# Optimization experiments

Measured on AMD Instinct MI355X. Metric: run time of the kernel, lower is better.

## Reference

```python
import jax, jax.numpy as jnp
import numpy as np

B, D_IN, HID, DIM, M = 4096, 128, 200, 256, 32
SIGMA, OMEGA = 1.0, 1.7
LB, UB = 0.0, 1.0


def setup_inputs() -> dict:
    key = jax.random.key(0)
    ks = jax.random.split(key, 9)
    s = lambda d: 1.0 / jnp.sqrt(jnp.float32(d))
    return {
        "x": jax.random.normal(ks[0], (B, D_IN), jnp.float32),
        "b": jax.random.uniform(ks[1], (B, M), jnp.float32),
        "W1": jax.random.normal(ks[2], (D_IN, HID), jnp.float32) * s(D_IN),
        "b1": jnp.zeros((HID,), jnp.float32),
        "W2": jax.random.normal(ks[3], (HID, HID), jnp.float32) * s(HID),
        "b2": jnp.zeros((HID,), jnp.float32),
        "W3": jax.random.normal(ks[4], (HID, DIM), jnp.float32) * s(HID),
        "b3": jnp.zeros((DIM,), jnp.float32),
        "A": jax.random.normal(ks[5], (M, DIM), jnp.float32) * s(DIM),
        "step": 1000,
        "n_iter": 100,
    }


def reference(x, b, W1, b1, W2, b2, W3, b3, A, step, n_iter):
    # --- MLP: Dense(200) -> relu -> Dense(200) -> relu -> Dense(dim) ---
    h = jax.nn.relu(x @ W1 + b1)
    h = jax.nn.relu(h @ W2 + b2)
    y = h @ W3 + b3  # [B, DIM]

    # schedule = linear_schedule(0.0, 0.0, ...) -> alpha == 0.0 always
    alpha = jnp.float32(0.0)

    # --- projection onto {z : A z = b, LB <= z <= UB} via relaxed
    # Douglas-Rachford / SOR fixed-point iteration (sigma/omega) ---
    AAt_inv = jnp.linalg.inv(A @ A.T + 1e-6 * jnp.eye(M, dtype=A.dtype))

    def p_aff(z):  # affine equality projection, z: [B, DIM]
        r = z @ A.T - b            # [B, M] residual
        return z - (r @ AAt_inv) @ A

    def p_box(z):
        return jnp.clip(z, LB, UB)

    def body(z, _):
        u = p_aff(z)
        v = p_box(2.0 * u - z)     # reflection then box projection
        z = z + SIGMA * OMEGA * (v - u)
        return z, None

    z0 = y  # project.get_init(x): initialize fixed point at MLP output
    z_final, _ = jax.lax.scan(body, z0, None, length=n_iter)
    proj = p_aff(z_final)

    # interpolation between raw MLP output and projection (alpha == 0)
    out = alpha * y + (1.0 - alpha) * proj
    return out
```

## Files before the change

### kernel.cpp

```cpp
#include <hip/hip_runtime.h>
#include <hip/hip_bf16.h>

typedef float    f4v    __attribute__((ext_vector_type(4)));
typedef short    short8 __attribute__((ext_vector_type(8)));
typedef unsigned u2v    __attribute__((ext_vector_type(2)));

constexpr int Bn = 4096, TR = 16;

__device__ inline unsigned cvt2(float x, float y) {
  union { __hip_bfloat162 h; unsigned u; } c;
  c.h = __float22bfloat162_rn(float2{x, y});
  return c.u;
}
__device__ inline void split_pair(float x, float y, unsigned& hp, unsigned& lp) {
  hp = cvt2(x, y);
  float hx = __uint_as_float(hp << 16);
  float hy = __uint_as_float(hp & 0xffff0000u);
  lp = cvt2(x - hx, y - hy);
}
union S8U { unsigned u[4]; short8 s; };
__device__ inline void split8(const float v[8], short8& hi, short8& lo) {
  S8U h, l;
  #pragma unroll
  for (int d = 0; d < 4; ++d) split_pair(v[2 * d], v[2 * d + 1], h.u[d], l.u[d]);
  hi = h.s; lo = l.s;
}
__device__ inline void split8p(const float* p, short8& hi, short8& lo) {
  f4v a = *(const f4v*)p, b = *(const f4v*)(p + 4);
  float v[8] = {a[0], a[1], a[2], a[3], b[0], b[1], b[2], b[3]};
  split8(v, hi, lo);
}
__device__ inline f4v mfma16(short8 a, short8 b, f4v c) {
  return __builtin_amdgcn_mfma_f32_16x16x32_bf16(a, b, c, 0, 0, 0);
}
__device__ __attribute__((always_inline)) inline f4v gdot8(
    const short8 (&ah)[8], const short8 (&al)[8],
    const short8 (&bh)[8], const short8 (&bl)[8]) {
  f4v c = {0.f, 0.f, 0.f, 0.f};
  #pragma unroll
  for (int s = 0; s < 8; ++s) {
    c = mfma16(ah[s], bh[s], c);
    c = mfma16(al[s], bh[s], c);
    c = mfma16(ah[s], bl[s], c);
  }
  return c;
}

__global__ __launch_bounds__(256) void k_prep(const float* __restrict__ A,
                                              float* __restrict__ KAT) {
  __shared__ __align__(16) float As[32 * 256];
  __shared__ float Gm[32 * 68];
  __shared__ float GinvL[32 * 32];

  const int t = threadIdx.x;
  const int lane = t & 63, wv = t >> 6, quad = lane >> 4, l15 = lane & 15;
  const int T = wv & 1, kh = wv >> 1;

  for (int i = t; i < 2048; i += 256)
    ((f4v*)As)[i] = ((const f4v*)A)[i];
  __syncthreads();

  {
    short8 afh[2][8], afl[2][8];
    #pragma unroll
    for (int tt = 0; tt < 2; ++tt)
      #pragma unroll
      for (int s = 0; s < 8; ++s)
        split8p(As + (l15 + 16 * tt) * 256 + 32 * s + 8 * quad,
                afh[tt][s], afl[tt][s]);
    f4v cg;
    if      (wv == 0) cg = gdot8(afh[0], afl[0], afh[0], afl[0]);
    else if (wv == 1) cg = gdot8(afh[1], afl[1], afh[0], afl[0]);
    else if (wv == 2) cg = gdot8(afh[0], afl[0], afh[1], afl[1]);
    else              cg = gdot8(afh[1], afl[1], afh[1], afl[1]);
    #pragma unroll
    for (int r = 0; r < 4; ++r) {
      int gi = 16 * T + 4 * quad + r, gj = 16 * kh + l15;
      Gm[gi * 68 + gj]      = cg[r] + (gi == gj ? 1e-6f : 0.f);
      Gm[gi * 68 + 32 + gj] = (gi == gj) ? 1.f : 0.f;
    }
  }
  __syncthreads();

  if (wv == 0) {
    float gcol[32];
    #pragma unroll
    for (int i = 0; i < 32; ++i) gcol[i] = Gm[i * 68 + lane];
    #pragma unroll
    for (int k = 0; k < 32; ++k) {
      float ckk  = __shfl(gcol[k], k);
      float ipiv = 1.f / ckk;
      float pivj = gcol[k] * ipiv;
      gcol[k] = pivj;
      #pragma unroll
      for (int i = 0; i < 32; ++i) {
        if (i == k) continue;
        float cki = __shfl(gcol[i], k);
        gcol[i] = fmaf(-cki, pivj, gcol[i]);
      }
    }
    if (lane >= 32) {
      #pragma unroll
      for (int i = 0; i < 32; ++i) GinvL[i * 32 + (lane - 32)] = gcol[i];
    }
  }
  __syncthreads();

  {
    float res[32];
    #pragma unroll
    for (int m = 0; m < 32; ++m) res[m] = 0.f;
    for (int p = 0; p < 32; ++p) {
      float av = As[p * 256 + t];
      #pragma unroll
      for (int m4 = 0; m4 < 8; ++m4) {
        f4v g = *(const f4v*)&GinvL[p * 32 + 4 * m4];
        res[4 * m4 + 0] = fmaf(av, g[0], res[4 * m4 + 0]);
        res[4 * m4 + 1] = fmaf(av, g[1], res[4 * m4 + 1]);
        res[4 * m4 + 2] = fmaf(av, g[2], res[4 * m4 + 2]);
        res[4 * m4 + 3] = fmaf(av, g[3], res[4 * m4 + 3]);
      }
    }
    #pragma unroll
    for (int m4 = 0; m4 < 8; ++m4) {
      f4v v = {res[4 * m4], res[4 * m4 + 1], res[4 * m4 + 2], res[4 * m4 + 3]};
      *(f4v*)&KAT[t * 32 + 4 * m4] = v;
    }
  }
}

__global__ __launch_bounds__(256, 1) void k_main(
    const float* __restrict__ x,  const float* __restrict__ bmat,
    const float* __restrict__ W1, const float* __restrict__ b1,
    const float* __restrict__ W2, const float* __restrict__ b2,
    const float* __restrict__ W3, const float* __restrict__ b3,
    const float* __restrict__ A,  const float* __restrict__ KAT,
    const int* __restrict__ n_iter_p, float* __restrict__ out) {

  __shared__ __align__(16) float smem[11328];

  const int t = threadIdx.x;
  const int lane = t & 63, wv = t >> 6, quad = lane >> 4, l15 = lane & 15;
  const int row0 = blockIdx.x * TR;

  float* xs = smem;
  float* h1 = smem + 2112;
  float* h2 = smem + 5440;
  float* ys = smem;
  unsigned* zsm = (unsigned*)smem;
  float* rb = smem + 8768 + wv * 640;

  {
    int r = t >> 4, c8 = t & 15;
    *(f4v*)&xs[r * 132 + 8 * c8]     = *(const f4v*)&x[(size_t)(row0 + r) * 128 + 8 * c8];
    *(f4v*)&xs[r * 132 + 8 * c8 + 4] = *(const f4v*)&x[(size_t)(row0 + r) * 128 + 8 * c8 + 4];
  }
  __syncthreads();

  {
    const int rg = wv, oc = lane;
    const bool g3 = (oc < 8);
    float acc[4][4];

    #pragma unroll
    for (int oi = 0; oi < 4; ++oi)
      #pragma unroll
      for (int r = 0; r < 4; ++r) acc[oi][r] = 0.f;
    for (int k4 = 0; k4 < 32; ++k4) {
      float xv[4][4];
      #pragma unroll
      for (int r = 0; r < 4; ++r) {
        f4v v = *(const f4v*)&xs[(4 * rg + r) * 132 + 4 * k4];
        xv[r][0] = v[0]; xv[r][1] = v[1]; xv[r][2] = v[2]; xv[r][3] = v[3];
      }
      #pragma unroll
      for (int kk = 0; kk < 4; ++kk) {
        const float* wr = W1 + (4 * k4 + kk) * 200 + oc;
        float w0 = wr[0], w1c = wr[64], w2c = wr[128];
        float w3c = g3 ? wr[192] : 0.f;
        #pragma unroll
        for (int r = 0; r < 4; ++r) {
          acc[0][r] = fmaf(xv[r][kk], w0, acc[0][r]);
          acc[1][r] = fmaf(xv[r][kk], w1c, acc[1][r]);
          acc[2][r] = fmaf(xv[r][kk], w2c, acc[2][r]);
          acc[3][r] = fmaf(xv[r][kk], w3c, acc[3][r]);
        }
      }
    }
    #pragma unroll
    for (int oi = 0; oi < 4; ++oi) {
      if (oi == 3 && !g3) continue;
      float bb = b1[oc + 64 * oi];
      #pragma unroll
      for (int r = 0; r < 4; ++r)
        h1[(4 * rg + r) * 208 + oc + 64 * oi] = fmaxf(acc[oi][r] + bb, 0.f);
    }
    __syncthreads();

    #pragma unroll
    for (int oi = 0; oi < 4; ++oi)
      #pragma unroll
      for (int r = 0; r < 4; ++r) acc[oi][r] = 0.f;
    for (int k4 = 0; k4 < 50; ++k4) {
      float xv[4][4];
      #pragma unroll
      for (int r = 0; r < 4; ++r) {
        f4v v = *(const f4v*)&h1[(4 * rg + r) * 208 + 4 * k4];
        xv[r][0] = v[0]; xv[r][1] = v[1]; xv[r][2] = v[2]; xv[r][3] = v[3];
      }
      #pragma unroll
      for (int kk = 0; kk < 4; ++kk) {
        const float* wr = W2 + (4 * k4 + kk) * 200 + oc;
        float w0 = wr[0], w1c = wr[64], w2c = wr[128];
        float w3c = g3 ? wr[192] : 0.f;
        #pragma unroll
        for (int r = 0; r < 4; ++r) {
          acc[0][r] = fmaf(xv[r][kk], w0, acc[0][r]);
          acc[1][r] = fmaf(xv[r][kk], w1c, acc[1][r]);
          acc[2][r] = fmaf(xv[r][kk], w2c, acc[2][r]);
          acc[3][r] = fmaf(xv[r][kk], w3c, acc[3][r]);
        }
      }
    }
    #pragma unroll
    for (int oi = 0; oi < 4; ++oi) {
      if (oi == 3 && !g3) continue;
      float bb = b2[oc + 64 * oi];
      #pragma unroll
      for (int r = 0; r < 4; ++r)
        h2[(4 * rg + r) * 208 + oc + 64 * oi] = fmaxf(acc[oi][r] + bb, 0.f);
    }
    __syncthreads();

    #pragma unroll
    for (int oi = 0; oi < 4; ++oi)
      #pragma unroll
      for (int r = 0; r < 4; ++r) acc[oi][r] = 0.f;
    for (int k4 = 0; k4 < 50; ++k4) {
      float xv[4][4];
      #pragma unroll
      for (int r = 0; r < 4; ++r) {
        f4v v = *(const f4v*)&h2[(4 * rg + r) * 208 + 4 * k4];
        xv[r][0] = v[0]; xv[r][1] = v[1]; xv[r][2] = v[2]; xv[r][3] = v[3];
      }
      #pragma unroll
      for (int kk = 0; kk < 4; ++kk) {
        const float* wr = W3 + (4 * k4 + kk) * 256 + oc;
        float w0 = wr[0], w1c = wr[64], w2c = wr[128], w3c = wr[192];
        #pragma unroll
        for (int r = 0; r < 4; ++r) {
          acc[0][r] = fmaf(xv[r][kk], w0, acc[0][r]);
          acc[1][r] = fmaf(xv[r][kk], w1c, acc[1][r]);
          acc[2][r] = fmaf(xv[r][kk], w2c, acc[2][r]);
          acc[3][r] = fmaf(xv[r][kk], w3c, acc[3][r]);
        }
      }
    }
    __syncthreads();
    #pragma unroll
    for (int oi = 0; oi < 4; ++oi) {
      float bb = b3[oc + 64 * oi];
      #pragma unroll
      for (int r = 0; r < 4; ++r)
        ys[(4 * rg + r) * 260 + oc + 64 * oi] = acc[oi][r] + bb;
    }
  }
  __syncthreads();

  short8 aah[2][8], aal[2][8];
  f4v binit[2];
  #pragma unroll
  for (int T = 0; T < 2; ++T) {
    #pragma unroll
    for (int s = 0; s < 8; ++s) {
      const float* ap = A + (size_t)(l15 + 16 * T) * 256 + 32 * s + 8 * quad;
      float v[8];
      #pragma unroll
      for (int j = 0; j < 8; ++j) v[j] = ap[j];
      split8(v, aah[T][s], aal[T][s]);
    }
    f4v bv = *(const f4v*)&bmat[(size_t)(row0 + l15) * 32 + 16 * T + 4 * quad];
    binit[T] = -bv;
  }

  short8 kanh[4], kanl[4];
  #pragma unroll
  for (int u = 0; u < 4; ++u) {
    const int U = 4 * wv + u;
    const float* kp = KAT + (size_t)(16 * U + l15) * 32 + 8 * quad;
    float v[8];
    #pragma unroll
    for (int j = 0; j < 8; ++j) v[j] = kp[j];
    split8(v, kanh[u], kanl[u]);
  }

  int zoff[4];
  #pragma unroll
  for (int u = 0; u < 4; ++u) {
    const int U = 4 * wv + u;
    const int qp = 2 * (U & 1) + (quad >> 1);
    zoff[u] = (((U >> 3) * 4 + ((U >> 1) & 3)) * 2) * 256
              + qp * 64 + l15 * 4 + 2 * (quad & 1);
  }

  float zr[4][4];
  #pragma unroll
  for (int u = 0; u < 4; ++u) {
    const int U = 4 * wv + u;
    f4v yv = *(const f4v*)&ys[l15 * 260 + 16 * U + 4 * quad];
    #pragma unroll
    for (int r = 0; r < 4; ++r) zr[u][r] = yv[r];
  }
  __syncthreads();
  #pragma unroll
  for (int u = 0; u < 4; ++u) {
    unsigned h0, l0, h1_, l1_;
    split_pair(zr[u][0], zr[u][1], h0, l0);
    split_pair(zr[u][2], zr[u][3], h1_, l1_);
    u2v hv; hv[0] = h0; hv[1] = h1_;
    u2v lv; lv[0] = l0; lv[1] = l1_;
    *(u2v*)&zsm[zoff[u]] = hv;
    *(u2v*)&zsm[zoff[u] + 256] = lv;
  }
  __syncthreads();

  const int niter = n_iter_p[0];
  int p = 0;

  for (int it = 0; it <= niter; ++it) {
    const unsigned* zb = zsm + p * 4096;

    f4v c0[2], c1[2];
    c0[0] = binit[0]; c0[1] = binit[1];
    c1[0] = f4v{0.f, 0.f, 0.f, 0.f};
    c1[1] = f4v{0.f, 0.f, 0.f, 0.f};
    #pragma unroll
    for (int half = 0; half < 2; ++half) {
      short8 zfh[4], zfl[4];
      #pragma unroll
      for (int q4 = 0; q4 < 4; ++q4) {
        int s = 4 * half + q4;
        zfh[q4] = *(const short8*)&zb[(s * 2 + 0) * 256 + lane * 4];
        zfl[q4] = *(const short8*)&zb[(s * 2 + 1) * 256 + lane * 4];
      }
      #pragma unroll
      for (int q4 = 0; q4 < 4; ++q4) {
        int s = 4 * half + q4;
        #pragma unroll
        for (int T = 0; T < 2; ++T) {
          f4v cc = (q4 & 1) ? c1[T] : c0[T];
          cc = mfma16(aah[T][s], zfh[q4], cc);
          cc = mfma16(aal[T][s], zfh[q4], cc);
          cc = mfma16(aah[T][s], zfl[q4], cc);
          if (q4 & 1) c1[T] = cc; else c0[T] = cc;
        }
      }
    }
    #pragma unroll
    for (int T = 0; T < 2; ++T) {
      f4v rA = c0[T] + c1[T];
      *(f4v*)&rb[l15 * 36 + 16 * T + 4 * quad] = rA;
    }
    f4v ra = *(const f4v*)&rb[l15 * 36 + 8 * quad];
    f4v rbv = *(const f4v*)&rb[l15 * 36 + 8 * quad + 4];
    float rv[8] = {ra[0], ra[1], ra[2], ra[3], rbv[0], rbv[1], rbv[2], rbv[3]};
    short8 rh, rl;
    split8(rv, rh, rl);

    f4v cB[4];
    #pragma unroll
    for (int u = 0; u < 4; ++u) {
      f4v cc = {0.f, 0.f, 0.f, 0.f};
      cc = mfma16(kanh[u], rh, cc);
      cc = mfma16(kanl[u], rh, cc);
      cc = mfma16(kanh[u], rl, cc);
      cB[u] = cc;
    }

    if (it < niter) {
      unsigned* zw = zsm + (p ^ 1) * 4096;
      #pragma unroll
      for (int u = 0; u < 4; ++u) {
        #pragma unroll
        for (int r = 0; r < 4; ++r) {
          float z = zr[u][r], wvv = cB[u][r];
          float vv = fminf(fmaxf(z - 2.f * wvv, 0.f), 1.f);
          zr[u][r] = fmaf(1.7f, vv - z + wvv, z);
        }
        unsigned h0, l0, h1_, l1_;
        split_pair(zr[u][0], zr[u][1], h0, l0);
        split_pair(zr[u][2], zr[u][3], h1_, l1_);
        u2v hv; hv[0] = h0; hv[1] = h1_;
        u2v lv; lv[0] = l0; lv[1] = l1_;
        *(u2v*)&zw[zoff[u]] = hv;
        *(u2v*)&zw[zoff[u] + 256] = lv;
      }
      __syncthreads();
      p ^= 1;
    } else {
      #pragma unroll
      for (int u = 0; u < 4; ++u) {
        const int U = 4 * wv + u;
        f4v ov;
        #pragma unroll
        for (int r = 0; r < 4; ++r) ov[r] = zr[u][r] - cB[u][r];
        *(f4v*)&out[(size_t)(row0 + l15) * 256 + 16 * U + 4 * quad] = ov;
      }
    }
  }
}

extern "C" void kernel_launch(void* const* d_in, const int* in_sizes, int n_in,
                              void* d_out, int out_size, void* d_ws, size_t ws_size,
                              hipStream_t stream) {
  const float* x    = (const float*)d_in[0];
  const float* bmat = (const float*)d_in[1];
  const float* W1   = (const float*)d_in[2];
  const float* b1   = (const float*)d_in[3];
  const float* W2   = (const float*)d_in[4];
  const float* b2   = (const float*)d_in[5];
  const float* W3   = (const float*)d_in[6];
  const float* b3   = (const float*)d_in[7];
  const float* A    = (const float*)d_in[8];
  const int*  n_it  = (const int*)d_in[10];
  float* KAT = (float*)d_ws;
  float* out = (float*)d_out;

  hipLaunchKernelGGL(k_prep, dim3(1), dim3(256), 0, stream, A, KAT);
  hipLaunchKernelGGL(k_main, dim3(Bn / TR), dim3(256), 0, stream,
                     x, bmat, W1, b1, W2, b2, W3, b3, A, KAT, n_it, out);
}
```

Before: 271.7 us.

## Run projection loop on a single wave with K fragments staged in LDS

Pre-splits the KAT matrix into bf16 hi/lo fragments in shared memory. After the MLP, only wave 0 continues, holding all 16 z tiles in registers and computing both projection GEMMs itself. This removes the per-iteration block barrier and the double-buffered z exchange. In exchange, one wave does all the second-GEMM MFMA work serially and the other three SIMDs sit idle during the loop.

```diff
diff --git a/kernel.cpp b/kernel.cpp
--- a/kernel.cpp
+++ b/kernel.cpp
@@ -4,6 +4,7 @@
 typedef float    f4v    __attribute__((ext_vector_type(4)));
 typedef short    short8 __attribute__((ext_vector_type(8)));
 typedef unsigned u2v    __attribute__((ext_vector_type(2)));
+typedef unsigned u4v    __attribute__((ext_vector_type(4)));
 
 constexpr int Bn = 4096, TR = 16;
 
@@ -18,7 +19,7 @@
   float hy = __uint_as_float(hp & 0xffff0000u);
   lp = cvt2(x - hx, y - hy);
 }
-union S8U { unsigned u[4]; short8 s; };
+union S8U { unsigned u[4]; short8 s; u4v v4; };
 __device__ inline void split8(const float v[8], short8& hi, short8& lo) {
   S8U h, l;
   #pragma unroll
@@ -137,18 +138,20 @@
     const float* __restrict__ A,  const float* __restrict__ KAT,
     const int* __restrict__ n_iter_p, float* __restrict__ out) {
 
-  __shared__ __align__(16) float smem[11328];
+  __shared__ __align__(16) float    ubuf[8768];
+  __shared__ __align__(16) unsigned zfrag[4096];
+  __shared__ __align__(16) unsigned kfh[4096];
+  __shared__ __align__(16) unsigned kfl[4096];
+  __shared__ __align__(16) float    rb[576];
 
   const int t = threadIdx.x;
   const int lane = t & 63, wv = t >> 6, quad = lane >> 4, l15 = lane & 15;
   const int row0 = blockIdx.x * TR;
 
-  float* xs = smem;
-  float* h1 = smem + 2112;
-  float* h2 = smem + 5440;
-  float* ys = smem;
-  unsigned* zsm = (unsigned*)smem;
-  float* rb = smem + 8768 + wv * 640;
+  float* xs = ubuf;
+  float* h1 = ubuf + 2112;
+  float* h2 = ubuf + 5440;
+  float* ys = ubuf;
 
   {
     int r = t >> 4, c8 = t & 15;
@@ -265,7 +268,23 @@
         ys[(4 * rg + r) * 260 + oc + 64 * oi] = acc[oi][r] + bb;
     }
   }
+
+  #pragma unroll
+  for (int u = 0; u < 4; ++u) {
+    const int U = 4 * wv + u;
+    float v[8];
+    #pragma unroll
+    for (int j = 0; j < 8; ++j)
+      v[j] = KAT[(size_t)(16 * U + l15) * 32 + 8 * quad + j];
+    S8U h, l;
+    #pragma unroll
+    for (int d = 0; d < 4; ++d) split_pair(v[2 * d], v[2 * d + 1], h.u[d], l.u[d]);
+    *(u4v*)&kfh[U * 256 + lane * 4] = h.v4;
+    *(u4v*)&kfl[U * 256 + lane * 4] = l.v4;
+  }
   __syncthreads();
+
+  if (wv != 0) return;
 
   short8 aah[2][8], aal[2][8];
   f4v binit[2];
@@ -283,127 +302,98 @@
     binit[T] = -bv;
   }
 
-  short8 kanh[4], kanl[4];
-  #pragma unroll
-  for (int u = 0; u < 4; ++u) {
-    const int U = 4 * wv + u;
-    const float* kp = KAT + (size_t)(16 * U + l15) * 32 + 8 * quad;
-    float v[8];
-    #pragma unroll
-    for (int j = 0; j < 8; ++j) v[j] = kp[j];
-    split8(v, kanh[u], kanl[u]);
-  }
-
-  int zoff[4];
-  #pragma unroll
-  for (int u = 0; u < 4; ++u) {
-    const int U = 4 * wv + u;
-    const int qp = 2 * (U & 1) + (quad >> 1);
-    zoff[u] = (((U >> 3) * 4 + ((U >> 1) & 3)) * 2) * 256
-              + qp * 64 + l15 * 4 + 2 * (quad & 1);
-  }
-
-  float zr[4][4];
-  #pragma unroll
-  for (int u = 0; u < 4; ++u) {
-    const int U = 4 * wv + u;
-    f4v yv = *(const f4v*)&ys[l15 * 260 + 16 * U + 4 * quad];
-    #pragma unroll
-    for (int r = 0; r < 4; ++r) zr[u][r] = yv[r];
-  }
-  __syncthreads();
-  #pragma unroll
-  for (int u = 0; u < 4; ++u) {
+  const int zlane = (quad >> 1) * 64 + l15 * 4 + 2 * (quad & 1);
+
+  f4v zr[16];
+  #pragma unroll
+  for (int U = 0; U < 16; ++U)
+    zr[U] = *(const f4v*)&ys[l15 * 260 + 16 * U + 4 * quad];
+  #pragma unroll
+  for (int U = 0; U < 16; ++U) {
+    const int zo = (((U >> 3) * 4 + ((U >> 1) & 3)) * 2) * 256 + (U & 1) * 128 + zlane;
     unsigned h0, l0, h1_, l1_;
-    split_pair(zr[u][0], zr[u][1], h0, l0);
-    split_pair(zr[u][2], zr[u][3], h1_, l1_);
+    split_pair(zr[U][0], zr[U][1], h0, l0);
+    split_pair(zr[U][2], zr[U][3], h1_, l1_);
     u2v hv; hv[0] = h0; hv[1] = h1_;
     u2v lv; lv[0] = l0; lv[1] = l1_;
-    *(u2v*)&zsm[zoff[u]] = hv;
-    *(u2v*)&zsm[zoff[u] + 256] = lv;
-  }
-  __syncthreads();
+    *(u2v*)&zfrag[zo] = hv;
+    *(u2v*)&zfrag[zo + 256] = lv;
+  }
 
   const int niter = n_iter_p[0];
-  int p = 0;
 
   for (int it = 0; it <= niter; ++it) {
-    const unsigned* zb = zsm + p * 4096;
+    short8 zfh[8], zfl[8];
+    #pragma unroll
+    for (int s = 0; s < 8; ++s) {
+      zfh[s] = *(const short8*)&zfrag[(s * 2 + 0) * 256 + lane * 4];
+      zfl[s] = *(const short8*)&zfrag[(s * 2 + 1) * 256 + lane * 4];
+    }
 
     f4v c0[2], c1[2];
     c0[0] = binit[0]; c0[1] = binit[1];
     c1[0] = f4v{0.f, 0.f, 0.f, 0.f};
     c1[1] = f4v{0.f, 0.f, 0.f, 0.f};
     #pragma unroll
-    for (int half = 0; half < 2; ++half) {
-      short8 zfh[4], zfl[4];
-      #pragma unroll
-      for (int q4 = 0; q4 < 4; ++q4) {
-        int s = 4 * half + q4;
-        zfh[q4] = *(const short8*)&zb[(s * 2 + 0) * 256 + lane * 4];
-        zfl[q4] = *(const short8*)&zb[(s * 2 + 1) * 256 + lane * 4];
-      }
-      #pragma unroll
-      for (int q4 = 0; q4 < 4; ++q4) {
-        int s = 4 * half + q4;
-        #pragma unroll
-        for (int T = 0; T < 2; ++T) {
-          f4v cc = (q4 & 1) ? c1[T] : c0[T];
-          cc = mfma16(aah[T][s], zfh[q4], cc);
-          cc = mfma16(aal[T][s], zfh[q4], cc);
-          cc = mfma16(aah[T][s], zfl[q4], cc);
-          if (q4 & 1) c1[T] = cc; else c0[T] = cc;
-        }
-      }
-    }
+    for (int s = 0; s < 8; ++s) {
+      #pragma unroll
+      for (int T = 0; T < 2; ++T) {
+        f4v cc = (s & 1) ? c1[T] : c0[T];
+        cc = mfma16(aah[T][s], zfh[s], cc);
+        cc = mfma16(aal[T][s], zfh[s], cc);
+        cc = mfma16(aah[T][s], zfl[s], cc);
+        if (s & 1) c1[T] = cc; else c0[T] = cc;
+      }
+    }
+
     #pragma unroll
     for (int T = 0; T < 2; ++T) {
       f4v rA = c0[T] + c1[T];
       *(f4v*)&rb[l15 * 36 + 16 * T + 4 * quad] = rA;
     }
-    f4v ra = *(const f4v*)&rb[l15 * 36 + 8 * quad];
+    f4v ra  = *(const f4v*)&rb[l15 * 36 + 8 * quad];
     f4v rbv = *(const f4v*)&rb[l15 * 36 + 8 * quad + 4];
     float rv[8] = {ra[0], ra[1], ra[2], ra[3], rbv[0], rbv[1], rbv[2], rbv[3]};
     short8 rh, rl;
     split8(rv, rh, rl);
 
-    f4v cB[4];
-    #pragma unroll
-    for (int u = 0; u < 4; ++u) {
-      f4v cc = {0.f, 0.f, 0.f, 0.f};
-      cc = mfma16(kanh[u], rh, cc);
-      cc = mfma16(kanl[u], rh, cc);
-      cc = mfma16(kanh[u], rl, cc);
-      cB[u] = cc;
-    }
-
     if (it < niter) {
-      unsigned* zw = zsm + (p ^ 1) * 4096;
-      #pragma unroll
-      for (int u = 0; u < 4; ++u) {
+      #pragma unroll
+      for (int U = 0; U < 16; ++U) {
+        short8 kh = *(const short8*)&kfh[U * 256 + lane * 4];
+        short8 kl = *(const short8*)&kfl[U * 256 + lane * 4];
+        f4v cc = {0.f, 0.f, 0.f, 0.f};
+        cc = mfma16(kh, rh, cc);
+        cc = mfma16(kl, rh, cc);
+        cc = mfma16(kh, rl, cc);
+        f4v z = zr[U];
         #pragma unroll
         for (int r = 0; r < 4; ++r) {
-          float z = zr[u][r], wvv = cB[u][r];
-          float vv = fminf(fmaxf(z - 2.f * wvv, 0.f), 1.f);
-          zr[u][r] = fmaf(1.7f, vv - z + wvv, z);
+          float vv = fminf(fmaxf(z[r] - 2.f * cc[r], 0.f), 1.f);
+          z[r] = fmaf(1.7f, vv - z[r] + cc[r], z[r]);
         }
+        zr[U] = z;
+        const int zo = (((U >> 3) * 4 + ((U >> 1) & 3)) * 2) * 256 + (U & 1) * 128 + zlane;
         unsigned h0, l0, h1_, l1_;
-        split_pair(zr[u][0], zr[u][1], h0, l0);
-        split_pair(zr[u][2], zr[u][3], h1_, l1_);
+        split_pair(z[0], z[1], h0, l0);
+        split_pair(z[2], z[3], h1_, l1_);
         u2v hv; hv[0] = h0; hv[1] = h1_;
         u2v lv; lv[0] = l0; lv[1] = l1_;
-        *(u2v*)&zw[zoff[u]] = hv;
-        *(u2v*)&zw[zoff[u] + 256] = lv;
-      }
-      __syncthreads();
-      p ^= 1;
+        *(u2v*)&zfrag[zo] = hv;
+        *(u2v*)&zfrag[zo + 256] = lv;
+      }
     } else {
       #pragma unroll
-      for (int u = 0; u < 4; ++u) {
-        const int U = 4 * wv + u;
+      for (int U = 0; U < 16; ++U) {
+        short8 kh = *(const short8*)&kfh[U * 256 + lane * 4];
+        short8 kl = *(const short8*)&kfl[U * 256 + lane * 4];
+        f4v cc = {0.f, 0.f, 0.f, 0.f};
+        cc = mfma16(kh, rh, cc);
+        cc = mfma16(kl, rh, cc);
+        cc = mfma16(kh, rl, cc);
         f4v ov;
         #pragma unroll
-        for (int r = 0; r < 4; ++r) ov[r] = zr[u][r] - cB[u][r];
+        for (int r = 0; r < 4; ++r) ov[r] = zr[U][r] - cc[r];
         *(f4v*)&out[(size_t)(row0 + l15) * 256 + 16 * U + 4 * quad] = ov;
       }
     }
```

Measured after the change: 388.0 us. +42.8%, slower.
